# Performance work log

Measured on AMD Instinct MI355X. Metric: run time of the kernel, lower is better.

The kernel has to match this reference:

```python
import jax, jax.numpy as jnp
import numpy as np

TOPK = 2
EPS = float(np.finfo(np.float64).eps)


def setup_inputs() -> dict:
    key = jax.random.key(0)
    ks = jax.random.split(key, 6)
    B, D, E = 8192, 1024, 8
    x = jax.random.normal(ks[0], (B, D), dtype=jnp.float32)
    noise = jax.random.normal(ks[1], (B, E), dtype=jnp.float32)
    w_gate = jax.random.normal(ks[2], (D, E), dtype=jnp.float32) * 0.02
    w_noise = jax.random.normal(ks[3], (D, E), dtype=jnp.float32) * 0.02
    W_experts = jax.random.normal(ks[4], (E, D, D), dtype=jnp.float32) * 0.02
    b_experts = jax.random.normal(ks[5], (E, D), dtype=jnp.float32) * 0.02
    return {"x": x, "noise": noise, "w_gate": w_gate, "w_noise": w_noise,
            "W_experts": W_experts, "b_experts": b_experts}


def _gates(x, w_gate, w_noise, noise):
    # noisy top-k gating (Shazeer et al.)
    clean_logits = x @ w_gate                                  # [B, E]
    noise_stddev = jax.nn.softplus(x @ w_noise) + 0.01         # [B, E]
    logits = clean_logits + noise * noise_stddev               # [B, E]
    E = logits.shape[1]
    top_logits, top_idx = jax.lax.top_k(logits, min(TOPK + 1, E))
    top_k_logits = top_logits[:, :TOPK]
    top_k_idx = top_idx[:, :TOPK]
    top_k_gates = jax.nn.softmax(top_k_logits, axis=1)         # [B, k]
    B = logits.shape[0]
    gates = jnp.zeros_like(logits).at[jnp.arange(B)[:, None], top_k_idx].set(top_k_gates)
    return gates                                               # [B, E] sparse


def reference(x, noise, w_gate, w_noise, W_experts, b_experts):
    gates = _gates(x, w_gate, w_noise, noise)                  # [B, E]
    # dense equivalent of sort-based dispatch/combine: zero gates mask out
    # unselected experts, so the combined result is identical math.
    expert_out = jnp.einsum("bd,edh->beh", x, W_experts) + b_experts[None]  # [B, E, D]
    combined = jnp.einsum("be,beh->bh", gates, jnp.exp(expert_out))         # [B, D]
    combined = jnp.where(combined == 0, EPS, combined)
    return jnp.log(combined)
```

## Files before the change

kernel.cpp:

```cpp
#include <hip/hip_runtime.h>
#include <hip/hip_bf16.h>
#include <math.h>

#define B_ROWS 8192
#define DDIM   1024
#define NEXP   8

typedef __attribute__((ext_vector_type(8))) __bf16 bf16x8;
typedef __attribute__((ext_vector_type(4))) float  f32x4;

__device__ __forceinline__ unsigned short f2bf(float f) {
    unsigned u = __builtin_bit_cast(unsigned, f);
    u = (u + 0x7fffu + ((u >> 16) & 1u)) >> 16;
    return (unsigned short)u;
}

#define GLOAD_LDS16(gptr, lptr)                                                \
    __builtin_amdgcn_global_load_lds(                                          \
        (const __attribute__((address_space(1))) unsigned int*)(gptr),         \
        (__attribute__((address_space(3))) unsigned int*)(lptr), 16, 0, 0)

__global__ __launch_bounds__(256) void xconv_kernel(
    const float* __restrict__ x, __hip_bfloat16* __restrict__ xbf)
{
    int i = blockIdx.x * 256 + threadIdx.x;
    const int stride = gridDim.x * 256;
    const int n8 = B_ROWS * DDIM / 8;
    for (; i < n8; i += stride) {
        const float4 f0 = *(const float4*)(x + (size_t)i * 8);
        const float4 f1 = *(const float4*)(x + (size_t)i * 8 + 4);
        union { bf16x8 v; unsigned short u[8]; } pk;
        pk.u[0] = f2bf(f0.x); pk.u[1] = f2bf(f0.y); pk.u[2] = f2bf(f0.z); pk.u[3] = f2bf(f0.w);
        pk.u[4] = f2bf(f1.x); pk.u[5] = f2bf(f1.y); pk.u[6] = f2bf(f1.z); pk.u[7] = f2bf(f1.w);
        *(bf16x8*)((__hip_bfloat16*)xbf + (size_t)i * 8) = pk.v;
    }
}

__global__ __launch_bounds__(256) void wtrans_kernel(
    const float* __restrict__ W, __hip_bfloat16* __restrict__ Wt)
{
    const int e  = blockIdx.z;
    const int k0 = blockIdx.y * 64;
    const int n0 = blockIdx.x * 64;
    __shared__ float st[64][65];

    const int t = threadIdx.x;
    {
        const int kk = t >> 4;
        const int nn = (t & 15) * 4;
#pragma unroll
        for (int p = 0; p < 4; ++p) {
            const int k = p * 16 + kk;
            const float4 v = *(const float4*)(W + (size_t)e * DDIM * DDIM
                                                + (size_t)(k0 + k) * DDIM + n0 + nn);
            st[k][nn + 0] = v.x; st[k][nn + 1] = v.y;
            st[k][nn + 2] = v.z; st[k][nn + 3] = v.w;
        }
    }
    __syncthreads();
    {
        const int wave = t >> 6, lane = t & 63;
        const int nr = lane >> 3, kc = lane & 7;
#pragma unroll
        for (int p = 0; p < 2; ++p) {
            const int n = p * 32 + wave * 8 + nr;
            union { bf16x8 v; unsigned short u[8]; } pk;
#pragma unroll
            for (int j = 0; j < 8; ++j) pk.u[j] = f2bf(st[kc * 8 + j][n]);
            *(bf16x8*)((__hip_bfloat16*)Wt + (size_t)e * DDIM * DDIM
                        + (size_t)(n0 + n) * DDIM + k0 + kc * 8) = pk.v;
        }
    }
}

__global__ __launch_bounds__(256) void wprep_kernel(
    const float* __restrict__ wg, const float* __restrict__ wn, float* __restrict__ wtr)
{
    const int idx = blockIdx.x * 256 + threadIdx.x;
    if (idx < 16 * DDIM) {
        const int k8  = idx >> 7;
        const int rem = idx & 127;
        const int c   = rem >> 3;
        const int j   = rem & 7;
        const int k   = k8 * 8 + j;
        wtr[idx] = (c < 8) ? wg[k * NEXP + c] : wn[k * NEXP + (c - 8)];
    }
}

__global__ __launch_bounds__(256) void gating_kernel(
    const float* __restrict__ x, const float* __restrict__ noise,
    const float* __restrict__ wtr,
    int* __restrict__ counts, int* __restrict__ rowlist, float* __restrict__ gatelist)
{
    const int t = threadIdx.x;
    const int wave = t >> 6, lane = t & 63;
    const int ks = lane >> 5;
    const int rs = (lane >> 4) & 1;
    const int c  = lane & 15;
    const int row = blockIdx.x * 8 + wave * 2 + rs;

    const float* xr = x   + (size_t)row * DDIM + ks * 512;
    const float* wr = wtr + (size_t)ks * 8192 + c * 8;

    double a0 = 0, a1 = 0, a2 = 0, a3 = 0, a4 = 0, a5 = 0, a6 = 0, a7 = 0;
    for (int ko = 0; ko < 16; ++ko) {
        float4 xb[8], wb[8];
#pragma unroll
        for (int i = 0; i < 4; ++i) {
            const int k8 = ko * 4 + i;
            xb[2 * i]     = *(const float4*)(xr + k8 * 8);
            xb[2 * i + 1] = *(const float4*)(xr + k8 * 8 + 4);
            wb[2 * i]     = *(const float4*)(wr + k8 * 128);
            wb[2 * i + 1] = *(const float4*)(wr + k8 * 128 + 4);
        }
#pragma unroll
        for (int i = 0; i < 4; ++i) {
            a0 += (double)(xb[2 * i].x     * wb[2 * i].x);
            a1 += (double)(xb[2 * i].y     * wb[2 * i].y);
            a2 += (double)(xb[2 * i].z     * wb[2 * i].z);
            a3 += (double)(xb[2 * i].w     * wb[2 * i].w);
            a4 += (double)(xb[2 * i + 1].x * wb[2 * i + 1].x);
            a5 += (double)(xb[2 * i + 1].y * wb[2 * i + 1].y);
            a6 += (double)(xb[2 * i + 1].z * wb[2 * i + 1].z);
            a7 += (double)(xb[2 * i + 1].w * wb[2 * i + 1].w);
        }
    }
    double acc = ((a0 + a1) + (a2 + a3)) + ((a4 + a5) + (a6 + a7));

    acc += __shfl_xor(acc, 32);

    const double vnoise = __shfl_xor(acc, 8);

    double lgv = -1.0e300;
    if (c < 8) {
        const double z  = vnoise;
        const double sp = (z > 30.0) ? z : log1p(exp(z));
        lgv = acc + (double)noise[(size_t)row * NEXP + c] * (sp + 0.01);
    }

    double bv = lgv; int bi = c;
#pragma unroll
    for (int off = 1; off <= 4; off <<= 1) {
        const double ov = __shfl_xor(bv, off);
        const int    oi = __shfl_xor(bi, off);
        if (ov > bv || (ov == bv && oi < bi)) { bv = ov; bi = oi; }
    }
    double b2v = (c == bi) ? -1.0e300 : lgv; int b2i = c;
#pragma unroll
    for (int off = 1; off <= 4; off <<= 1) {
        const double ov = __shfl_xor(b2v, off);
        const int    oi = __shfl_xor(b2i, off);
        if (ov > b2v || (ov == b2v && oi < b2i)) { b2v = ov; b2i = oi; }
    }

    if ((lane & 47) == 0) {
        const double g0 = 1.0 / (1.0 + exp(b2v - bv));
        const double g1 = 1.0 - g0;
        int p0 = atomicAdd(&counts[bi], 1);
        rowlist [bi * B_ROWS + p0] = row;
        gatelist[bi * B_ROWS + p0] = (float)g0;
        int p1 = atomicAdd(&counts[b2i], 1);
        rowlist [b2i * B_ROWS + p1] = (int)((unsigned)row | 0x80000000u);
        gatelist[b2i * B_ROWS + p1] = (float)g1;
    }
}

__global__ __launch_bounds__(256) void moe_gemm_kernel(
    const __hip_bfloat16* __restrict__ xbf, const __hip_bfloat16* __restrict__ Wt,
    const float* __restrict__ bias,
    const int* __restrict__ counts, const int* __restrict__ rowlist,
    const float* __restrict__ gatelist, float* __restrict__ out, float* __restrict__ out2)
{
    const int nt = blockIdx.x;
    const int e  = blockIdx.y;
    const int mt = blockIdx.z;
    const int cnt  = counts[e];
    const int row0 = mt * 128;
    if (row0 >= cnt) return;

    __shared__ int   srow[128];
    __shared__ unsigned char srank[128];
    __shared__ float sgate[128];
    __shared__ __align__(16) unsigned char Alds[128 * 128];
    __shared__ __align__(16) unsigned char Blds[128 * 128];

    const int t = threadIdx.x;
    if (t < 128) {
        const int r = row0 + t;
        const unsigned er = (r < cnt) ? (unsigned)rowlist[e * B_ROWS + r] : 0u;
        srow[t]  = (int)(er & 0x7fffffffu);
        srank[t] = (unsigned char)(er >> 31);
        sgate[t] = (r < cnt) ? gatelist[e * B_ROWS + r] : 0.0f;
    }
    __syncthreads();

    const int wave = t >> 6, lane = t & 63;
    const int wr = wave >> 1, wc = wave & 1;
    const int l4 = lane >> 4, l16 = lane & 15;
    const int lrow  = lane >> 3;
    const int lchunk = (lane & 7) ^ lrow;

    const char* asrc[4]; const char* bsrc[4];
#pragma unroll
    for (int i = 0; i < 4; ++i) {
        const int r  = wave * 32 + i * 8 + lrow;
        asrc[i] = (const char*)xbf + 2 * ((size_t)srow[r] * DDIM + lchunk * 8);
        const int gn = nt * 128 + wave * 32 + i * 8 + lrow;
        bsrc[i] = (const char*)Wt  + 2 * ((size_t)e * DDIM * DDIM + (size_t)gn * DDIM + lchunk * 8);
    }

    f32x4 acc[4][4];
#pragma unroll
    for (int m = 0; m < 4; ++m)
#pragma unroll
        for (int n = 0; n < 4; ++n) acc[m][n] = (f32x4){0.f, 0.f, 0.f, 0.f};

    for (int kt = 0; kt < DDIM / 64; ++kt) {
        const int koff = kt * 128;
#pragma unroll
        for (int i = 0; i < 4; ++i) {
            GLOAD_LDS16(asrc[i] + koff, Alds + (wave * 32 + i * 8) * 128);
            GLOAD_LDS16(bsrc[i] + koff, Blds + (wave * 32 + i * 8) * 128);
        }
        asm volatile("s_waitcnt vmcnt(0)" ::: "memory");
        __syncthreads();

#pragma unroll
        for (int ks = 0; ks < 2; ++ks) {
            bf16x8 af[4], bfr[4];
#pragma unroll
            for (int m = 0; m < 4; ++m) {
                const int row = wr * 64 + m * 16 + l16;
                af[m] = *(const bf16x8*)(Alds + row * 128 + ((ks * 64 + l4 * 16) ^ ((row & 7) << 4)));
            }
#pragma unroll
            for (int n = 0; n < 4; ++n) {
                const int rn = wc * 64 + n * 16 + l16;
                bfr[n] = *(const bf16x8*)(Blds + rn * 128 + ((ks * 64 + l4 * 16) ^ ((rn & 7) << 4)));
            }
#pragma unroll
            for (int m = 0; m < 4; ++m)
#pragma unroll
                for (int n = 0; n < 4; ++n)
                    acc[m][n] = __builtin_amdgcn_mfma_f32_16x16x32_bf16(af[m], bfr[n], acc[m][n], 0, 0, 0);
        }
        __syncthreads();
    }

#pragma unroll
    for (int m = 0; m < 4; ++m) {
#pragma unroll
        for (int n = 0; n < 4; ++n) {
#pragma unroll
            for (int j = 0; j < 4; ++j) {
                const int R = wr * 64 + m * 16 + l4 * 4 + j;
                if (row0 + R < cnt) {
                    const int   brow = srow[R];
                    const float g    = sgate[R];
                    const int   h    = nt * 128 + wc * 64 + n * 16 + l16;
                    const float v    = g * __expf(acc[m][n][j] + bias[e * DDIM + h]);
                    float* dst = srank[R] ? out2 : out;
                    dst[(size_t)brow * DDIM + h] = v;
                }
            }
        }
    }
}

__global__ __launch_bounds__(256) void logeps_kernel(
    float* __restrict__ o, const float* __restrict__ o2, int n4)
{
    const float EPSF = 2.220446049250313e-16f;
    int i = blockIdx.x * blockDim.x + threadIdx.x;
    const int stride = gridDim.x * blockDim.x;
    float4* p = (float4*)o;
    const float4* q = (const float4*)o2;
    for (; i < n4; i += stride) {
        float4 a = p[i];
        const float4 b = q[i];
        a.x += b.x; a.y += b.y; a.z += b.z; a.w += b.w;
        a.x = __logf(a.x == 0.0f ? EPSF : a.x);
        a.y = __logf(a.y == 0.0f ? EPSF : a.y);
        a.z = __logf(a.z == 0.0f ? EPSF : a.z);
        a.w = __logf(a.w == 0.0f ? EPSF : a.w);
        p[i] = a;
    }
}

extern "C" void kernel_launch(void* const* d_in, const int* in_sizes, int n_in,
                              void* d_out, int out_size, void* d_ws, size_t ws_size,
                              hipStream_t stream)
{
    const float* x       = (const float*)d_in[0];
    const float* noise   = (const float*)d_in[1];
    const float* w_gate  = (const float*)d_in[2];
    const float* w_noise = (const float*)d_in[3];
    const float* W       = (const float*)d_in[4];
    const float* bias    = (const float*)d_in[5];
    float* out = (float*)d_out;

    char* ws = (char*)d_ws;
    int*   counts   = (int*)ws;
    float* wtr      = (float*)(ws + 256);
    int*   rowlist  = (int*)(ws + 256 + 65536);
    float* gatelist = (float*)(ws + 256 + 65536 + NEXP * B_ROWS * 4);
    __hip_bfloat16* xbf = (__hip_bfloat16*)(ws + (1u << 20));
    __hip_bfloat16* Wt  = (__hip_bfloat16*)(ws + (1u << 20) + (16u << 20));
    float* out2 = (float*)(ws + (1u << 20) + (32u << 20));

    hipMemsetAsync(counts, 0, 64, stream);

    wprep_kernel<<<64, 256, 0, stream>>>(w_gate, w_noise, wtr);
    gating_kernel<<<B_ROWS / 8, 256, 0, stream>>>(x, noise, wtr,
                                                  counts, rowlist, gatelist);
    xconv_kernel<<<1024, 256, 0, stream>>>(x, xbf);
    wtrans_kernel<<<dim3(16, 16, NEXP), 256, 0, stream>>>(W, Wt);

    dim3 grid(NEXP , NEXP , B_ROWS / 128 );
    moe_gemm_kernel<<<grid, 256, 0, stream>>>(xbf, Wt, bias, counts, rowlist, gatelist,
                                              out, out2);

    logeps_kernel<<<2048, 256, 0, stream>>>(out, out2, out_size / 4);
}
```

Before: 364.8 us.

## Replace atomic expert binning with deterministic ballot-based bin kernel

The gating kernel now writes each row's two chosen experts and gate weights to per-row arrays instead of atomically appending to per-expert lists. A new single-block kernel scans all rows with one wave per expert, using ballots and popcounts to build ordered row and gate lists, and writes the counts itself, so the memset is no longer needed. This removes the global atomics, keeps the row lists sorted so GEMM gathers have better locality, and makes the ordering deterministic. The cost is an extra launch and a serial single-block scan over 8192 rows.

```diff
diff --git a/kernel.cpp b/kernel.cpp
--- a/kernel.cpp
+++ b/kernel.cpp
@@ -90,7 +90,7 @@
 __global__ __launch_bounds__(256) void gating_kernel(
     const float* __restrict__ x, const float* __restrict__ noise,
     const float* __restrict__ wtr,
-    int* __restrict__ counts, int* __restrict__ rowlist, float* __restrict__ gatelist)
+    int* __restrict__ ch, float2* __restrict__ gg)
 {
     const int t = threadIdx.x;
     const int wave = t >> 6, lane = t & 63;
@@ -155,14 +155,43 @@
 
     if ((lane & 47) == 0) {
         const double g0 = 1.0 / (1.0 + exp(b2v - bv));
-        const double g1 = 1.0 - g0;
-        int p0 = atomicAdd(&counts[bi], 1);
-        rowlist [bi * B_ROWS + p0] = row;
-        gatelist[bi * B_ROWS + p0] = (float)g0;
-        int p1 = atomicAdd(&counts[b2i], 1);
-        rowlist [b2i * B_ROWS + p1] = (int)((unsigned)row | 0x80000000u);
-        gatelist[b2i * B_ROWS + p1] = (float)g1;
-    }
+        ch[row] = bi | (b2i << 8);
+        gg[row] = make_float2((float)g0, (float)(1.0 - g0));
+    }
+}
+
+__global__ __launch_bounds__(512) void bin_kernel(
+    const int* __restrict__ ch, const float2* __restrict__ gg,
+    int* __restrict__ counts, int* __restrict__ rowlist, float* __restrict__ gatelist)
+{
+    const int e    = threadIdx.x >> 6;
+    const int lane = threadIdx.x & 63;
+    const unsigned long long ltmask = (1ull << lane) - 1ull;
+
+    int base = 0;
+    for (int chunk = 0; chunk < B_ROWS / 64; ++chunk) {
+        const int row = chunk * 64 + lane;
+        const int cv  = ch[row];
+        const int e0  = cv & 255;
+        const int e1  = (cv >> 8) & 255;
+        const bool h0 = (e0 == e);
+        const bool h1 = (e1 == e);
+        const unsigned long long m0 = __ballot(h0);
+        const unsigned long long m1 = __ballot(h1);
+        const int n0 = __popcll(m0);
+        if (h0) {
+            const int pos = base + __popcll(m0 & ltmask);
+            rowlist [e * B_ROWS + pos] = row;
+            gatelist[e * B_ROWS + pos] = gg[row].x;
+        }
+        if (h1) {
+            const int pos = base + n0 + __popcll(m1 & ltmask);
+            rowlist [e * B_ROWS + pos] = (int)((unsigned)row | 0x80000000u);
+            gatelist[e * B_ROWS + pos] = gg[row].y;
+        }
+        base += n0 + __popcll(m1);
+    }
+    if (lane == 0) counts[e] = base;
 }
 
 __global__ __launch_bounds__(256) void moe_gemm_kernel(
@@ -300,21 +329,21 @@
     float* out = (float*)d_out;
 
     char* ws = (char*)d_ws;
-    int*   counts   = (int*)ws;
-    float* wtr      = (float*)(ws + 256);
-    int*   rowlist  = (int*)(ws + 256 + 65536);
-    float* gatelist = (float*)(ws + 256 + 65536 + NEXP * B_ROWS * 4);
+    int*    counts   = (int*)ws;
+    float*  wtr      = (float*)(ws + 256);
+    int*    rowlist  = (int*)(ws + 65792);
+    float*  gatelist = (float*)(ws + 327936);
+    int*    ch       = (int*)(ws + 590080);
+    float2* gg       = (float2*)(ws + 622848);
     __hip_bfloat16* xbf = (__hip_bfloat16*)(ws + (1u << 20));
     __hip_bfloat16* Wt  = (__hip_bfloat16*)(ws + (1u << 20) + (16u << 20));
     float* out2 = (float*)(ws + (1u << 20) + (32u << 20));
 
-    hipMemsetAsync(counts, 0, 64, stream);
-
     wprep_kernel<<<64, 256, 0, stream>>>(w_gate, w_noise, wtr);
-    gating_kernel<<<B_ROWS / 8, 256, 0, stream>>>(x, noise, wtr,
-                                                  counts, rowlist, gatelist);
+    gating_kernel<<<B_ROWS / 8, 256, 0, stream>>>(x, noise, wtr, ch, gg);
     xconv_kernel<<<1024, 256, 0, stream>>>(x, xbf);
     wtrans_kernel<<<dim3(16, 16, NEXP), 256, 0, stream>>>(W, Wt);
+    bin_kernel<<<1, 512, 0, stream>>>(ch, gg, counts, rowlist, gatelist);
 
     dim3 grid(NEXP , NEXP , B_ROWS / 128 );
     moe_gemm_kernel<<<grid, 256, 0, stream>>>(xbf, Wt, bias, counts, rowlist, gatelist,
```

After: 345.5 us. -5.3%, faster.
